# Performance work log

Hardware: AMD Instinct MI355X
Metric: run time of the kernel (lower is better)

Reference implementation:

```python
import jax, jax.numpy as jnp
import numpy as np
from jax import lax

INPUT_DIM = 1024
DICT_SIZE = 16384
K = 32
BATCH = 4096


def setup_inputs() -> dict:
    key = jax.random.key(0)
    k1, k2, k3 = jax.random.split(key, 3)
    x = jax.random.normal(k1, (BATCH, INPUT_DIM), dtype=jnp.float32)
    # kaiming-uniform-ish init for encoder
    bound_enc = float(np.sqrt(6.0 / INPUT_DIM))
    W_enc = jax.random.uniform(k2, (DICT_SIZE, INPUT_DIM), dtype=jnp.float32,
                               minval=-bound_enc, maxval=bound_enc)
    b_enc = jnp.zeros((DICT_SIZE,), dtype=jnp.float32)
    bound_dec = float(np.sqrt(6.0 / DICT_SIZE))
    W_dec = jax.random.uniform(k3, (INPUT_DIM, DICT_SIZE), dtype=jnp.float32,
                               minval=-bound_dec, maxval=bound_dec)
    # normalize decoder columns to unit norm (dim=0), as in _init_weights
    W_dec = W_dec / (jnp.linalg.norm(W_dec, axis=0, keepdims=True) + 1e-12)
    b_dec = jnp.zeros((INPUT_DIM,), dtype=jnp.float32)
    return {"x": x, "W_enc": W_enc, "b_enc": b_enc, "W_dec": W_dec, "b_dec": b_dec}


def reference(x, W_enc, b_enc, W_dec, b_dec):
    batch = x.shape[0]
    # encode: F.linear(x - b_dec, W_enc, b_enc)
    pre_acts = jnp.einsum('bi,di->bd', x - b_dec, W_enc) + b_enc  # [B, D]
    relu_acts = jnp.maximum(pre_acts, 0.0)
    # batch top-k: keep top (k * batch) activations globally
    flat = relu_acts.reshape(-1)
    total_k = min(K * batch, flat.shape[0])
    top_vals, _ = lax.top_k(flat, total_k)
    threshold = top_vals[-1]  # == kthvalue(numel - total_k + 1)
    features = relu_acts * (relu_acts >= threshold).astype(relu_acts.dtype)
    # decode: F.linear(features, W_dec, b_dec)
    reconstructed = jnp.einsum('bd,id->bi', features, W_dec) + b_dec  # [B, I]
    diff = reconstructed - x
    reconstruction_loss = jnp.mean(diff * diff)
    sparsity_loss = jnp.asarray(0.0, dtype=x.dtype)
    loss = reconstruction_loss
    l0 = jnp.mean(jnp.sum((features > 0).astype(jnp.float32), axis=-1))
    return (reconstructed, features, loss, reconstruction_loss, sparsity_loss, l0)
```

## Files before the change

### kernel.cpp

```cpp
#include <hip/hip_runtime.h>
#include <cstdint>
#include <cstddef>

#define BATCH   4096
#define INDIM   1024
#define DICT    16384
#define TOTK    (32 * 4096)
#define NFEAT   ((size_t)BATCH * DICT)
#define DELTA   3e-2f
#define BAND    0.2f
#define PS_RANK (TOTK / 32)

#define NB2       4096
#define FBINS     2048
#define HCOPIES   64
#define CAND_CAP  (1u << 19)
#define BCAP      256u
#define ZLOC_CAP  2048u
#define CLOC_CAP  3072
#define C2_CAP    65536u
#define HASH_SZ   32768u
#define ROW_CAP   512
#define ZBINS     2048

#define PSH_OFF   0ull
#define FH_OFF    16384ull
#define SCAL_OFF  32768ull
#define H1_OFF    36864ull
#define ROWC_OFF  40960ull
#define HASH_OFF  65536ull
#define FBH_OFF   524288ull
#define MEMSET0   1572864ull
#define CANDI_OFF (2ull << 20)
#define CANDB_OFF (4ull << 20)
#define C2I_OFF   (6ull << 20)
#define C2V_OFF   ((6ull << 20) + 262144)
#define ENT_OFF   (7ull << 20)
#define AHI_OFF   (24ull << 20)
#define BHI_OFF   (32ull << 20)
#define WT_OFF    (24ull << 20)
#define WS_NEED   (88ull << 20)

typedef __attribute__((ext_vector_type(8))) short short8;
typedef __attribute__((ext_vector_type(4))) float f32x4;

#define GL2LDS16(g, l) __builtin_amdgcn_global_load_lds( \
    (const __attribute__((address_space(1))) void*)(g), \
    (__attribute__((address_space(3))) void*)(l), 16, 0, 0)

__device__ inline ushort bf16_rne_u(float a) {
    unsigned u = __float_as_uint(a);
    return (ushort)((u + 0x7FFFu + ((u >> 16) & 1u)) >> 16);
}

__device__ inline float bf16_to_f(ushort u) {
    return __uint_as_float(((unsigned)u) << 16);
}

__device__ inline int fshift_calc(unsigned BL, unsigned BH) {
    const unsigned range = BH - BL;
    int s = 0;
    while ((range >> s) > (unsigned)FBINS) ++s;
    return s;
}

__global__ __launch_bounds__(256) void split_kernel(
    const float* __restrict__ x, const float* __restrict__ W,
    const float* __restrict__ b_dec,
    ushort* __restrict__ Ahi, ushort* __restrict__ Bhi)
{
    const size_t NA = (size_t)BATCH * INDIM / 4;
    const size_t NB = (size_t)DICT * INDIM / 4;
    const size_t stride = (size_t)gridDim.x * blockDim.x;
    for (size_t i = (size_t)blockIdx.x * blockDim.x + threadIdx.x; i < NA + NB; i += stride) {
        float4 v;
        ushort* hp;
        if (i < NA) {
            v = reinterpret_cast<const float4*>(x)[i];
            const float4 bd = reinterpret_cast<const float4*>(b_dec)[i & (INDIM / 4 - 1)];
            v.x -= bd.x; v.y -= bd.y; v.z -= bd.z; v.w -= bd.w;
            hp = Ahi + i * 4;
        } else {
            v = reinterpret_cast<const float4*>(W)[i - NA];
            hp = Bhi + (i - NA) * 4;
        }
        ushort4 h;
        h.x = bf16_rne_u(v.x);
        h.y = bf16_rne_u(v.y);
        h.z = bf16_rne_u(v.z);
        h.w = bf16_rne_u(v.w);
        *reinterpret_cast<ushort4*>(hp) = h;
    }
}

__global__ __launch_bounds__(256) void presample_mfma(
    const ushort* __restrict__ Ahi, const ushort* __restrict__ Bhi,
    const float* __restrict__ b_enc, unsigned* __restrict__ pshist)
{
    __shared__ __align__(16) ushort As[128 * 64];
    __shared__ __align__(16) ushort Bs[128 * 64];
    __shared__ unsigned hls[NB2];
    const int tid = threadIdx.x;
    const int lane = tid & 63, wid = tid >> 6;
    const int n0 = blockIdx.x * 128;
    const int m0 = 0;
    const int wm = wid >> 1, wn = wid & 1;

    for (int i = tid; i < NB2; i += 256) hls[i] = 0;

    f32x4 acc[4][4];
#pragma unroll
    for (int i = 0; i < 4; ++i)
#pragma unroll
        for (int j = 0; j < 4; ++j) acc[i][j] = (f32x4){0.f, 0.f, 0.f, 0.f};

    const int srow = wid * 8 + (lane >> 3);
    const int schunk = (lane & 7) ^ (lane >> 3);
    const size_t abase = (size_t)(m0 + srow) * INDIM + schunk * 8;
    const size_t bbase = (size_t)(n0 + srow) * INDIM + schunk * 8;

    for (int t = 0; t < 16; ++t) {
        const int koff = t * 64;
#pragma unroll
        for (int i = 0; i < 4; ++i) {
            GL2LDS16(Ahi + abase + koff + (size_t)i * 32 * INDIM, &As[(i * 32 + wid * 8) * 64]);
            GL2LDS16(Bhi + bbase + koff + (size_t)i * 32 * INDIM, &Bs[(i * 32 + wid * 8) * 64]);
        }
        __syncthreads();
#pragma unroll
        for (int kq2 = 0; kq2 < 2; ++kq2) {
            short8 af[4], bf[4];
#pragma unroll
            for (int f = 0; f < 4; ++f) {
                const int ra = wm * 64 + f * 16 + (lane & 15);
                const int ca = (kq2 * 4 + (lane >> 4)) ^ (ra & 7);
                af[f] = *reinterpret_cast<const short8*>(&As[ra * 64 + ca * 8]);
                const int rb = wn * 64 + f * 16 + (lane & 15);
                const int cb = (kq2 * 4 + (lane >> 4)) ^ (rb & 7);
                bf[f] = *reinterpret_cast<const short8*>(&Bs[rb * 64 + cb * 8]);
            }
#pragma unroll
            for (int fm = 0; fm < 4; ++fm)
#pragma unroll
                for (int fn = 0; fn < 4; ++fn)
                    acc[fm][fn] = __builtin_amdgcn_mfma_f32_16x16x32_bf16(
                        af[fm], bf[fn], acc[fm][fn], 0, 0, 0);
        }
        __syncthreads();
    }

    const int ccol0 = n0 + wn * 64;
#pragma unroll
    for (int fm = 0; fm < 4; ++fm) {
#pragma unroll
        for (int fn = 0; fn < 4; ++fn) {
            const int col = ccol0 + fn * 16 + (lane & 15);
            const float be = b_enc[col];
#pragma unroll
            for (int r = 0; r < 4; ++r) {
                const float val = fmaxf(acc[fm][fn][r] + be, 0.f);
                if (val > 0.f) atomicAdd(&hls[__float_as_uint(val) >> 19], 1u);
            }
        }
    }
    __syncthreads();
    for (int i = tid; i < NB2; i += 256)
        if (hls[i]) atomicAdd(&pshist[i], hls[i]);
}

__global__ __launch_bounds__(1024) void presample_find(const unsigned* __restrict__ pshist,
                                                       unsigned* __restrict__ scal)
{
    __shared__ unsigned tot[NB2];
    __shared__ unsigned tsum[1024];
    __shared__ unsigned suffix[1024];
    const int t = threadIdx.x;
    unsigned s = 0;
#pragma unroll
    for (int i = 0; i < 4; ++i) {
        const int b = t * 4 + i;
        const unsigned v = pshist[b];
        tot[b] = v;
        s += v;
    }
    tsum[t] = s;
    __syncthreads();
    if (t == 0) {
        unsigned run = 0;
        for (int i = 1023; i >= 0; --i) { suffix[i] = run; run += tsum[i]; }
    }
    __syncthreads();
    unsigned cum = suffix[t];
    for (int i = 3; i >= 0; --i) {
        const unsigned b = (unsigned)(t * 4 + i);
        const unsigned nb = cum + tot[b];
        if (cum < PS_RANK && nb >= PS_RANK) {
            const float blo = __uint_as_float(b << 19);
            const float bhi = __uint_as_float((b + 1) << 19);
            scal[20] = __float_as_uint(fmaxf(blo - BAND, 1e-30f));
            scal[21] = __float_as_uint(bhi + BAND);
        }
        cum = nb;
    }
}

__global__ __launch_bounds__(256) void encode_main(
    const ushort* __restrict__ Ahi, const ushort* __restrict__ Bhi,
    const float* __restrict__ b_enc, unsigned* __restrict__ scal,
    unsigned* __restrict__ fhist, unsigned* __restrict__ candI,
    unsigned* __restrict__ candB)
{
    __shared__ __align__(16) ushort As[128 * 64];
    __shared__ __align__(16) ushort Bs[128 * 64];
    __shared__ unsigned ci[BCAP];
    __shared__ unsigned cb[BCAP];
    __shared__ unsigned lcnt, labv, sbase;
    const int tid = threadIdx.x;
    const int lane = tid & 63, wid = tid >> 6;
    const int flat = blockIdx.y * gridDim.x + blockIdx.x;
    const int n0 = ((flat & 7) * 16 + ((flat >> 3) & 15)) * 128;
    const int m0 = (flat >> 7) * 128;
    const int wm = wid >> 1, wn = wid & 1;

    if (tid == 0) { lcnt = 0; labv = 0; }

    const unsigned BLb = scal[20], BHb = scal[21];
    const float BLf = __uint_as_float(BLb);
    const int fs = fshift_calc(BLb, BHb);

    f32x4 acc[4][4];
#pragma unroll
    for (int i = 0; i < 4; ++i)
#pragma unroll
        for (int j = 0; j < 4; ++j) acc[i][j] = (f32x4){0.f, 0.f, 0.f, 0.f};

    const int srow = wid * 8 + (lane >> 3);
    const int schunk = (lane & 7) ^ (lane >> 3);
    const size_t abase = (size_t)(m0 + srow) * INDIM + schunk * 8;
    const size_t bbase = (size_t)(n0 + srow) * INDIM + schunk * 8;

    for (int t = 0; t < 16; ++t) {
        const int koff = t * 64;
#pragma unroll
        for (int i = 0; i < 4; ++i) {
            GL2LDS16(Ahi + abase + koff + (size_t)i * 32 * INDIM, &As[(i * 32 + wid * 8) * 64]);
            GL2LDS16(Bhi + bbase + koff + (size_t)i * 32 * INDIM, &Bs[(i * 32 + wid * 8) * 64]);
        }
        __syncthreads();
#pragma unroll
        for (int kq2 = 0; kq2 < 2; ++kq2) {
            short8 af[4], bf[4];
#pragma unroll
            for (int f = 0; f < 4; ++f) {
                const int ra = wm * 64 + f * 16 + (lane & 15);
                const int ca = (kq2 * 4 + (lane >> 4)) ^ (ra & 7);
                af[f] = *reinterpret_cast<const short8*>(&As[ra * 64 + ca * 8]);
                const int rb = wn * 64 + f * 16 + (lane & 15);
                const int cbx = (kq2 * 4 + (lane >> 4)) ^ (rb & 7);
                bf[f] = *reinterpret_cast<const short8*>(&Bs[rb * 64 + cbx * 8]);
            }
#pragma unroll
            for (int fm = 0; fm < 4; ++fm)
#pragma unroll
                for (int fn = 0; fn < 4; ++fn)
                    acc[fm][fn] = __builtin_amdgcn_mfma_f32_16x16x32_bf16(
                        af[fm], bf[fn], acc[fm][fn], 0, 0, 0);
        }
        __syncthreads();
    }

    const int crow0 = m0 + wm * 64;
    const int ccol0 = n0 + wn * 64;
#pragma unroll
    for (int fm = 0; fm < 4; ++fm) {
#pragma unroll
        for (int fn = 0; fn < 4; ++fn) {
            const int col = ccol0 + fn * 16 + (lane & 15);
            const float be = b_enc[col];
#pragma unroll
            for (int r = 0; r < 4; ++r) {
                const int row = crow0 + fm * 16 + (lane >> 4) * 4 + r;
                const float val = fmaxf(acc[fm][fn][r] + be, 0.f);
                if (val >= BLf) {
                    const unsigned u = __float_as_uint(val);
                    if (u < BHb) atomicAdd(&fhist[min((u - BLb) >> fs, (unsigned)(FBINS - 1))], 1u);
                    else atomicAdd(&labv, 1u);
                    const unsigned p = atomicAdd(&lcnt, 1u);
                    if (p < BCAP) {
                        ci[p] = (unsigned)(row * DICT + col);
                        cb[p] = u;
                    }
                }
            }
        }
    }
    __syncthreads();
    if (tid == 0) {
        if (labv) atomicAdd(&scal[16], labv);
        const unsigned n = min(lcnt, BCAP);
        if (lcnt > BCAP) atomicExch(&scal[17], 1u);
        sbase = atomicAdd(&scal[2], n);
    }
    __syncthreads();
    const unsigned n = min(lcnt, BCAP);
    const unsigned gb = sbase;
    for (unsigned k = tid; k < n; k += 256) {
        const unsigned g = gb + k;
        if (g < CAND_CAP) { candI[g] = ci[k]; candB[g] = cb[k]; }
        else atomicExch(&scal[17], 1u);
    }
}

__global__ __launch_bounds__(1024) void findfine_a(const unsigned* __restrict__ fhist,
                                                   unsigned* __restrict__ scal)
{
    __shared__ unsigned fhl[FBINS];
    __shared__ unsigned tsum[1024];
    __shared__ unsigned suffix[1024];
    __shared__ unsigned sfb;
    const int t = threadIdx.x;
    fhl[t * 2] = fhist[t * 2];
    fhl[t * 2 + 1] = fhist[t * 2 + 1];
    tsum[t] = fhl[t * 2] + fhl[t * 2 + 1];
    if (t == 0) sfb = 0xFFFFFFFFu;
    __syncthreads();
    if (t == 0) {
        unsigned run = 0;
        for (int i = 1023; i >= 0; --i) { suffix[i] = run; run += tsum[i]; }
    }
    __syncthreads();
    const unsigned aboveBH = scal[16];
    unsigned cum = aboveBH + suffix[t];
    {
        const unsigned b1 = (unsigned)(t * 2 + 1);
        unsigned nb = cum + fhl[b1];
        if (cum < TOTK && nb >= TOTK) sfb = b1;
        cum = nb;
        const unsigned b0 = (unsigned)(t * 2);
        nb = cum + fhl[b0];
        if (cum < TOTK && nb >= TOTK) sfb = b0;
    }
    __syncthreads();
    if (t == 0) {
        const unsigned BLb = scal[20], BHb = scal[21];
        bool ok = (sfb != 0xFFFFFFFFu) && (scal[17] == 0u) && (scal[2] <= CAND_CAP);
        if (ok) {
            const int fs = fshift_calc(BLb, BHb);
            const unsigned flo = BLb + (sfb << fs);
            const unsigned fhi = BLb + ((sfb + 1u) << fs) - 1u;
            const float zLo = __uint_as_float(flo) - DELTA;
            const float zHi = __uint_as_float(fhi) + DELTA;
            const unsigned ZL = __float_as_uint(fmaxf(zLo, 1e-30f));
            const unsigned ZH = __float_as_uint(zHi);
            ok = ok && (ZL >= BLb);
            scal[6] = ZL;
            scal[7] = ZH;
        }
        scal[18] = ok ? 1u : 0u;
    }
}

__global__ __launch_bounds__(256) void findfine_b(const unsigned* __restrict__ candB,
                                                  const unsigned* __restrict__ candI,
                                                  unsigned* __restrict__ scal,
                                                  unsigned* __restrict__ c2idx)
{
    if (!scal[18]) return;
    __shared__ unsigned lz[ZLOC_CAP];
    __shared__ unsigned red[256];
    __shared__ unsigned lcnt, sbase;
    const int tid = threadIdx.x;
    if (tid == 0) lcnt = 0;
    __syncthreads();
    const unsigned ZL = scal[6], ZH = scal[7];
    const unsigned C = min(scal[2], CAND_CAP);
    const unsigned stride = gridDim.x * blockDim.x;
    unsigned above = 0;
    for (unsigned i = blockIdx.x * blockDim.x + tid; i < C; i += stride) {
        const unsigned u = candB[i];
        if (u > ZH) above++;
        else if (u >= ZL) {
            const unsigned p = atomicAdd(&lcnt, 1u);
            if (p < ZLOC_CAP) lz[p] = candI[i];
        }
    }
    red[tid] = above;
    __syncthreads();
    for (int s = 128; s; s >>= 1) {
        if (tid < s) red[tid] += red[tid + s];
        __syncthreads();
    }
    if (tid == 0) {
        if (red[0]) atomicAdd(&scal[8], red[0]);
        const unsigned n = min(lcnt, ZLOC_CAP);
        if (lcnt > ZLOC_CAP) { atomicExch(&scal[17], 1u); atomicExch(&scal[18], 0u); }
        sbase = atomicAdd(&scal[9], n);
    }
    __syncthreads();
    const unsigned n = min(lcnt, ZLOC_CAP);
    const unsigned gb = sbase;
    for (unsigned k = tid; k < n; k += 256) {
        const unsigned g = gb + k;
        if (g < C2_CAP) c2idx[g] = lz[k];
        else { atomicExch(&scal[17], 1u); atomicExch(&scal[18], 0u); }
    }
}

__global__ __launch_bounds__(256) void fb_encode(
    const ushort* __restrict__ Ahi, const ushort* __restrict__ Bhi,
    const float* __restrict__ b_enc, float* __restrict__ feat,
    unsigned* __restrict__ fbhist, const unsigned* __restrict__ scal)
{
    if (scal[18]) return;
    __shared__ __align__(16) ushort As[128 * 64];
    __shared__ __align__(16) ushort Bs[128 * 64];
    __shared__ unsigned hls[NB2];
    const int tid = threadIdx.x;
    const int lane = tid & 63, wid = tid >> 6;
    const int flat = blockIdx.y * gridDim.x + blockIdx.x;
    const int swz = (flat & 7) * 512 + (flat >> 3);
    const int n0 = (swz & 127) * 128;
    const int m0 = (swz >> 7) * 128;
    const int wm = wid >> 1, wn = wid & 1;

    for (int i = tid; i < NB2; i += 256) hls[i] = 0;

    f32x4 acc[4][4];
#pragma unroll
    for (int i = 0; i < 4; ++i)
#pragma unroll
        for (int j = 0; j < 4; ++j) acc[i][j] = (f32x4){0.f, 0.f, 0.f, 0.f};

    const int srow = wid * 8 + (lane >> 3);
    const int schunk = (lane & 7) ^ (lane >> 3);
    const size_t abase = (size_t)(m0 + srow) * INDIM + schunk * 8;
    const size_t bbase = (size_t)(n0 + srow) * INDIM + schunk * 8;

    for (int t = 0; t < 16; ++t) {
        const int koff = t * 64;
#pragma unroll
        for (int i = 0; i < 4; ++i) {
            GL2LDS16(Ahi + abase + koff + (size_t)i * 32 * INDIM, &As[(i * 32 + wid * 8) * 64]);
            GL2LDS16(Bhi + bbase + koff + (size_t)i * 32 * INDIM, &Bs[(i * 32 + wid * 8) * 64]);
        }
        __syncthreads();
#pragma unroll
        for (int kq2 = 0; kq2 < 2; ++kq2) {
            short8 af[4], bf[4];
#pragma unroll
            for (int f = 0; f < 4; ++f) {
                const int ra = wm * 64 + f * 16 + (lane & 15);
                const int ca = (kq2 * 4 + (lane >> 4)) ^ (ra & 7);
                af[f] = *reinterpret_cast<const short8*>(&As[ra * 64 + ca * 8]);
                const int rb = wn * 64 + f * 16 + (lane & 15);
                const int cb = (kq2 * 4 + (lane >> 4)) ^ (rb & 7);
                bf[f] = *reinterpret_cast<const short8*>(&Bs[rb * 64 + cb * 8]);
            }
#pragma unroll
            for (int fm = 0; fm < 4; ++fm)
#pragma unroll
                for (int fn = 0; fn < 4; ++fn)
                    acc[fm][fn] = __builtin_amdgcn_mfma_f32_16x16x32_bf16(
                        af[fm], bf[fn], acc[fm][fn], 0, 0, 0);
        }
        __syncthreads();
    }

    const int crow0 = m0 + wm * 64;
    const int ccol0 = n0 + wn * 64;
#pragma unroll
    for (int fm = 0; fm < 4; ++fm) {
#pragma unroll
        for (int fn = 0; fn < 4; ++fn) {
            const int col = ccol0 + fn * 16 + (lane & 15);
            const float be = b_enc[col];
#pragma unroll
            for (int r = 0; r < 4; ++r) {
                const int row = crow0 + fm * 16 + (lane >> 4) * 4 + r;
                const float val = fmaxf(acc[fm][fn][r] + be, 0.f);
                feat[(size_t)row * DICT + col] = val;
                if (val > 0.f) atomicAdd(&hls[__float_as_uint(val) >> 19], 1u);
            }
        }
    }
    __syncthreads();
    unsigned* hdst = fbhist + (size_t)(flat & (HCOPIES - 1)) * NB2;
    for (int i = tid; i < NB2; i += 256)
        if (hls[i]) atomicAdd(&hdst[i], hls[i]);
}

__global__ __launch_bounds__(1024) void fb_findbin2(const unsigned* __restrict__ fbhist,
                                                    unsigned* __restrict__ scal)
{
    if (scal[18]) return;
    __shared__ unsigned tot[NB2];
    __shared__ unsigned tsum[1024];
    __shared__ unsigned suffix[1024];
    const int t = threadIdx.x;
    if (t == 0) { scal[9] = 0; scal[8] = 0; }
    unsigned s = 0;
#pragma unroll
    for (int i = 0; i < 4; ++i) {
        const int b = t * 4 + i;
        unsigned v = 0;
        for (int c = 0; c < HCOPIES; ++c) v += fbhist[(size_t)c * NB2 + b];
        tot[b] = v;
        s += v;
    }
    tsum[t] = s;
    __syncthreads();
    if (t == 0) {
        unsigned run = 0;
        for (int i = 1023; i >= 0; --i) { suffix[i] = run; run += tsum[i]; }
    }
    __syncthreads();
    unsigned cum = suffix[t];
    for (int i = 3; i >= 0; --i) {
        const unsigned b = (unsigned)(t * 4 + i);
        const unsigned nb = cum + tot[b];
        if (cum < TOTK && nb >= TOTK) {
            scal[0] = b;
            scal[1] = cum;
            scal[10] = cum - ((b + 1 < NB2) ? tot[b + 1] : 0u);
        }
        cum = nb;
    }
}

__global__ __launch_bounds__(256) void fb_collectC(const float* __restrict__ feat,
                                                   unsigned* __restrict__ scal,
                                                   unsigned* __restrict__ candI,
                                                   unsigned* __restrict__ candB,
                                                   unsigned* __restrict__ h1)
{
    if (scal[18]) return;
    __shared__ unsigned lidx[CLOC_CAP];
    __shared__ unsigned lbits[CLOC_CAP];
    __shared__ unsigned lcnt;
    __shared__ unsigned sbase;
    const int tid = threadIdx.x;
    if (tid == 0) lcnt = 0;
    __syncthreads();
    const unsigned b = scal[0];
    const unsigned lob = (b > 0 ? b - 1 : b) << 19;
    const unsigned hib = ((b + 2 < NB2) ? (b + 2) : NB2) << 19;
    const size_t stride = (size_t)gridDim.x * blockDim.x * 4;
    size_t base = ((size_t)blockIdx.x * blockDim.x + tid) * 4;
    for (size_t i = base; i < NFEAT; i += stride) {
        const float4 v = *reinterpret_cast<const float4*>(&feat[i]);
        const unsigned u[4] = {__float_as_uint(v.x), __float_as_uint(v.y),
                               __float_as_uint(v.z), __float_as_uint(v.w)};
#pragma unroll
        for (int q = 0; q < 4; ++q) {
            if (u[q] != 0u && u[q] >= lob && u[q] < hib) {
                const unsigned p = atomicAdd(&lcnt, 1u);
                if (p < CLOC_CAP) { lidx[p] = (unsigned)(i + q); lbits[p] = u[q]; }
                if ((u[q] >> 19) == b) atomicAdd(&h1[(u[q] >> 9) & 1023u], 1u);
            }
        }
    }
    __syncthreads();
    const unsigned n = min(lcnt, (unsigned)CLOC_CAP);
    if (tid == 0) sbase = atomicAdd(&scal[24], n);
    __syncthreads();
    const unsigned gb = sbase;
    for (unsigned k = tid; k < n; k += 256) {
        const unsigned g = gb + k;
        if (g < CAND_CAP) { candI[g] = lidx[k]; candB[g] = lbits[k]; }
    }
}

__global__ __launch_bounds__(1024) void fb_selectZ(const unsigned* __restrict__ h1,
                                                   const unsigned* __restrict__ candB,
                                                   const unsigned* __restrict__ candI,
                                                   unsigned* __restrict__ scal,
                                                   unsigned* __restrict__ c2idx)
{
    if (scal[18]) return;
    __shared__ unsigned h[1024];
    __shared__ unsigned cnt[1024];
    const int t = threadIdx.x;
    h[t] = h1[t];
    __syncthreads();
    if (t == 0) {
        const unsigned b = scal[0];
        unsigned cum = scal[1];
        unsigned s = 0;
        for (int i = 1023; i >= 0; --i) {
            const unsigned nb = cum + h[i];
            if (cum < TOTK && nb >= TOTK) s = (unsigned)i;
            cum = nb;
        }
        const float slo = __uint_as_float((b << 19) | (s << 9));
        const float shi = __uint_as_float((b << 19) | (s << 9) | 0x1FFu);
        scal[6] = __float_as_uint(fmaxf(slo - DELTA, 1e-30f));
        scal[7] = __float_as_uint(shi + DELTA);
    }
    __syncthreads();
    const float ZLf = __uint_as_float(scal[6]);
    const float ZHf = __uint_as_float(scal[7]);
    const unsigned C = min(scal[24], CAND_CAP);
    unsigned above = 0;
    for (unsigned i = t; i < C; i += 1024) {
        const float v = __uint_as_float(candB[i]);
        if (v > ZHf) above++;
        else if (v >= ZLf) {
            const unsigned p = atomicAdd(&scal[9], 1u);
            if (p < C2_CAP) c2idx[p] = candI[i];
        }
    }
    cnt[t] = above;
    __syncthreads();
    for (int s2 = 512; s2; s2 >>= 1) {
        if (t < s2) cnt[t] += cnt[t + s2];
        __syncthreads();
    }
    if (t == 0) scal[8] = scal[10] + cnt[0];
}

__global__ __launch_bounds__(256) void refine2_kernel(
    const float* __restrict__ x, const float* __restrict__ W,
    const float* __restrict__ b_enc, const float* __restrict__ b_dec,
    const unsigned* __restrict__ scal, const unsigned* __restrict__ c2idx,
    float* __restrict__ c2val)
{
    const unsigned n = min(scal[9], C2_CAP);
    const size_t stride = (size_t)gridDim.x * blockDim.x;
    for (unsigned c = blockIdx.x * blockDim.x + threadIdx.x; c < n; c += stride) {
        const unsigned i = c2idx[c];
        const int m = (int)(i >> 14);
        const int d = (int)(i & (DICT - 1));
        const float* xr = x + (size_t)m * INDIM;
        const float* wr = W + (size_t)d * INDIM;
        const int kb[4] = {0, 384, 704, 1024};
        float tot = 0.f;
        for (int p = 0; p < 3; ++p) {
            float a = 0.f;
#pragma unroll 8
            for (int k = kb[p]; k < kb[p + 1]; ++k)
                a = fmaf(xr[k] - b_dec[k], wr[k], a);
            tot = (p == 0) ? a : (tot + a);
        }
        c2val[c] = tot + b_enc[d];
    }
}

__device__ inline int zone_shift(unsigned ZL, unsigned ZH) {
    const unsigned range = ZH - ZL + 1u;
    int shift = 0;
    while ((range >> shift) > (unsigned)ZBINS) ++shift;
    return shift;
}

__global__ __launch_bounds__(1024) void findv_kernel(const float* __restrict__ c2val,
                                                     unsigned* __restrict__ scal)
{
    __shared__ unsigned h[ZBINS];
    __shared__ float mem[1024];
    __shared__ unsigned mcnt;
    __shared__ unsigned sbsel, sjj;
    const int t = threadIdx.x;
    h[t] = 0;
    h[t + 1024] = 0;
    if (t == 0) mcnt = 0;
    __syncthreads();
    const unsigned n = min(scal[9], C2_CAP);
    const unsigned ZL = scal[6], ZH = scal[7];
    const int shift = zone_shift(ZL, ZH);
    for (unsigned i = t; i < n; i += 1024) {
        const unsigned bits = __float_as_uint(c2val[i]);
        const unsigned idx = (bits <= ZL) ? 0u : min((unsigned)(ZBINS - 1), (bits - ZL) >> shift);
        atomicAdd(&h[idx], 1u);
    }
    __syncthreads();
    unsigned j = TOTK - scal[8];
    if (j > n) j = n;
    if (t == 0) {
        unsigned cum = 0, bsel = 0, jj = j;
        for (int i = ZBINS - 1; i >= 0; --i) {
            const unsigned nb = cum + h[i];
            if (cum < j && nb >= j) { bsel = (unsigned)i; jj = j - cum; }
            cum = nb;
        }
        sbsel = bsel; sjj = jj;
    }
    __syncthreads();
    const unsigned bsel = sbsel, jj = sjj;
    for (unsigned i = t; i < n; i += 1024) {
        const unsigned bits = __float_as_uint(c2val[i]);
        const unsigned idx = (bits <= ZL) ? 0u : min((unsigned)(ZBINS - 1), (bits - ZL) >> shift);
        if (idx == bsel) {
            const unsigned p = atomicAdd(&mcnt, 1u);
            if (p < 1024) mem[p] = c2val[i];
        }
    }
    __syncthreads();
    const unsigned m = min(mcnt, 1024u);
    for (unsigned i = t; i < m; i += 1024) {
        const float v = mem[i];
        unsigned g = 0, eq = 0;
        for (unsigned d = 0; d < m; ++d) {
            g += (mem[d] > v) ? 1u : 0u;
            eq += (mem[d] == v) ? 1u : 0u;
        }
        if (g < jj && g + eq >= jj) scal[11] = __float_as_uint(v);
    }
}

__global__ __launch_bounds__(256) void keephash_kernel(const unsigned* __restrict__ scal,
                                                       const unsigned* __restrict__ c2idx,
                                                       const float* __restrict__ c2val,
                                                       uint2* __restrict__ hash)
{
    const unsigned n = min(scal[9], C2_CAP);
    const float vj = __uint_as_float(scal[11]);
    const unsigned stride = gridDim.x * blockDim.x;
    for (unsigned i = blockIdx.x * blockDim.x + threadIdx.x; i < n; i += stride) {
        const float v = c2val[i];
        if (v >= vj) {
            const unsigned key = c2idx[i];
            unsigned s = (key * 2654435761u) & (HASH_SZ - 1);
            while (atomicCAS(&hash[s].x, 0xFFFFFFFFu, key) != 0xFFFFFFFFu)
                s = (s + 1) & (HASH_SZ - 1);
            hash[s].y = __float_as_uint(v);
        }
    }
}

__global__ void transpose_kernel(const float* __restrict__ W, ushort* __restrict__ Wt)
{
    __shared__ float t[32][33];
    const int x0 = blockIdx.x * 32;
    const int y0 = blockIdx.y * 32;
    const int tx = threadIdx.x, ty = threadIdx.y;
    for (int r = ty; r < 32; r += 8)
        t[r][tx] = W[(size_t)(y0 + r) * DICT + x0 + tx];
    __syncthreads();
    for (int r = ty; r < 32; r += 8)
        Wt[(size_t)(x0 + r) * INDIM + y0 + tx] = bf16_rne_u(t[tx][r]);
}

__global__ __launch_bounds__(256) void scatter_kernel(
    unsigned* __restrict__ scal, const unsigned* __restrict__ candI,
    const unsigned* __restrict__ candB, const uint2* __restrict__ hash,
    float* __restrict__ feat, uint2* __restrict__ entries,
    unsigned* __restrict__ rowcnt)
{
    if (!scal[18]) return;
    __shared__ unsigned red[256];
    const unsigned C = min(scal[2], CAND_CAP);
    const unsigned ZL = scal[6], ZH = scal[7];
    const unsigned stride = gridDim.x * blockDim.x;
    unsigned kept = 0;
    for (unsigned i = blockIdx.x * blockDim.x + threadIdx.x; i < C; i += stride) {
        const unsigned u = candB[i];
        const unsigned idx = candI[i];
        float val = 0.f;
        bool keep = false;
        if (u > ZH) {
            val = __uint_as_float(u);
            keep = true;
        } else if (u >= ZL) {
            unsigned s = (idx * 2654435761u) & (HASH_SZ - 1);
            while (true) {
                const uint2 e = hash[s];
                if (e.x == idx) { val = __uint_as_float(e.y); keep = true; break; }
                if (e.x == 0xFFFFFFFFu) break;
                s = (s + 1) & (HASH_SZ - 1);
            }
        }
        if (keep) {
            feat[idx] = val;
            const unsigned row = idx >> 14;
            const unsigned p = atomicAdd(&rowcnt[row], 1u);
            if (p < ROW_CAP)
                entries[(size_t)row * ROW_CAP + p] =
                    make_uint2(idx & (DICT - 1), __float_as_uint(val));
            kept++;
        }
    }
    red[threadIdx.x] = kept;
    __syncthreads();
    for (int s = 128; s; s >>= 1) {
        if (threadIdx.x < s) red[threadIdx.x] += red[threadIdx.x + s];
        __syncthreads();
    }
    if (threadIdx.x == 0 && red[0]) atomicAdd(&scal[4], red[0]);
}

__global__ __launch_bounds__(256) void decode2_kernel(
    const unsigned* __restrict__ scal, const uint2* __restrict__ entries,
    const unsigned* __restrict__ rowcnt, const ushort* __restrict__ Wt,
    const float* __restrict__ b_dec, const float* __restrict__ x,
    float* __restrict__ recon, double* __restrict__ loss_sum)
{
    if (!scal[18]) return;
    __shared__ uint2 lst[ROW_CAP];
    __shared__ double redd[256];
    const int row = blockIdx.x;
    const int tid = threadIdx.x;
    const unsigned n = min(rowcnt[row], (unsigned)ROW_CAP);
    for (unsigned i = tid; i < n; i += 256) lst[i] = entries[(size_t)row * ROW_CAP + i];
    __syncthreads();
    float4 acc = make_float4(0.f, 0.f, 0.f, 0.f);
    for (unsigned e = 0; e < n; ++e) {
        const uint2 en = lst[e];
        const float v = __uint_as_float(en.y);
        const ushort4 w4 = *reinterpret_cast<const ushort4*>(Wt + (size_t)en.x * INDIM + tid * 4);
        acc.x = fmaf(v, bf16_to_f(w4.x), acc.x);
        acc.y = fmaf(v, bf16_to_f(w4.y), acc.y);
        acc.z = fmaf(v, bf16_to_f(w4.z), acc.z);
        acc.w = fmaf(v, bf16_to_f(w4.w), acc.w);
    }
    const float4 bd = reinterpret_cast<const float4*>(b_dec)[tid];
    acc.x += bd.x; acc.y += bd.y; acc.z += bd.z; acc.w += bd.w;
    reinterpret_cast<float4*>(recon + (size_t)row * INDIM)[tid] = acc;
    const float4 xv = reinterpret_cast<const float4*>(x + (size_t)row * INDIM)[tid];
    const double d0 = (double)acc.x - (double)xv.x;
    const double d1 = (double)acc.y - (double)xv.y;
    const double d2 = (double)acc.z - (double)xv.z;
    const double d3 = (double)acc.w - (double)xv.w;
    redd[tid] = d0 * d0 + d1 * d1 + d2 * d2 + d3 * d3;
    __syncthreads();
    for (int s = 128; s; s >>= 1) {
        if (tid < s) redd[tid] += redd[tid + s];
        __syncthreads();
    }
    if (tid == 0) atomicAdd(loss_sum, redd[0]);
}

__global__ __launch_bounds__(256) void fb_compact_decode(
    float* __restrict__ feat, unsigned* __restrict__ scal,
    const uint2* __restrict__ hash, const ushort* __restrict__ Wt,
    const float* __restrict__ b_dec, const float* __restrict__ x,
    float* __restrict__ recon, double* __restrict__ loss_sum)
{
    if (scal[18]) return;
    __shared__ uint2 lst[ROW_CAP];
    __shared__ unsigned cnt;
    __shared__ double redd[256];
    const int row = blockIdx.x;
    const int tid = threadIdx.x;
    if (tid == 0) cnt = 0;
    __syncthreads();
    const float ZLf = __uint_as_float(scal[6]);
    const float ZHf = __uint_as_float(scal[7]);
    float* frow = feat + (size_t)row * DICT;
#pragma unroll
    for (int it = 0; it < DICT / 4 / 256; ++it) {
        const int i4 = it * 256 + tid;
        float4 v = reinterpret_cast<float4*>(frow)[i4];
        float a[4] = {v.x, v.y, v.z, v.w};
        float out[4] = {0.f, 0.f, 0.f, 0.f};
#pragma unroll
        for (int q = 0; q < 4; ++q) {
            const float val = a[q];
            if (val > ZHf) {
                out[q] = val;
            } else if (val >= ZLf && val > 0.f) {
                const unsigned key = (unsigned)(row * DICT + i4 * 4 + q);
                unsigned s = (key * 2654435761u) & (HASH_SZ - 1);
                while (true) {
                    const uint2 e = hash[s];
                    if (e.x == key) { out[q] = __uint_as_float(e.y); break; }
                    if (e.x == 0xFFFFFFFFu) break;
                    s = (s + 1) & (HASH_SZ - 1);
                }
            }
            if (out[q] != 0.f) {
                const unsigned p = atomicAdd(&cnt, 1u);
                if (p < ROW_CAP)
                    lst[p] = make_uint2((unsigned)(i4 * 4 + q), __float_as_uint(out[q]));
            }
        }
        reinterpret_cast<float4*>(frow)[i4] = make_float4(out[0], out[1], out[2], out[3]);
    }
    __syncthreads();
    const unsigned n = min(cnt, (unsigned)ROW_CAP);
    float4 acc = make_float4(0.f, 0.f, 0.f, 0.f);
    for (unsigned e = 0; e < n; ++e) {
        const uint2 en = lst[e];
        const float v = __uint_as_float(en.y);
        const ushort4 w4 = *reinterpret_cast<const ushort4*>(Wt + (size_t)en.x * INDIM + tid * 4);
        acc.x = fmaf(v, bf16_to_f(w4.x), acc.x);
        acc.y = fmaf(v, bf16_to_f(w4.y), acc.y);
        acc.z = fmaf(v, bf16_to_f(w4.z), acc.z);
        acc.w = fmaf(v, bf16_to_f(w4.w), acc.w);
    }
    const float4 bd = reinterpret_cast<const float4*>(b_dec)[tid];
    acc.x += bd.x; acc.y += bd.y; acc.z += bd.z; acc.w += bd.w;
    reinterpret_cast<float4*>(recon + (size_t)row * INDIM)[tid] = acc;
    const float4 xv = reinterpret_cast<const float4*>(x + (size_t)row * INDIM)[tid];
    const double d0 = (double)acc.x - (double)xv.x;
    const double d1 = (double)acc.y - (double)xv.y;
    const double d2 = (double)acc.z - (double)xv.z;
    const double d3 = (double)acc.w - (double)xv.w;
    redd[tid] = d0 * d0 + d1 * d1 + d2 * d2 + d3 * d3;
    __syncthreads();
    for (int s = 128; s; s >>= 1) {
        if (tid < s) redd[tid] += redd[tid + s];
        __syncthreads();
    }
    if (tid == 0) {
        atomicAdd(loss_sum, redd[0]);
        if (cnt) atomicAdd(&scal[4], cnt);
    }
}

__global__ void finalize_kernel(const unsigned* __restrict__ scal, float* __restrict__ tail)
{
    const double* loss_d = reinterpret_cast<const double*>(&scal[12]);
    const float rec = (float)(loss_d[0] / (double)((size_t)BATCH * INDIM));
    tail[0] = rec;
    tail[1] = rec;
    tail[2] = 0.f;
    tail[3] = (float)scal[4] / (float)BATCH;
}

extern "C" void kernel_launch(void* const* d_in, const int* in_sizes, int n_in,
                              void* d_out, int out_size, void* d_ws, size_t ws_size,
                              hipStream_t stream)
{
    const float* x     = (const float*)d_in[0];
    const float* W_enc = (const float*)d_in[1];
    const float* b_enc = (const float*)d_in[2];
    const float* W_dec = (const float*)d_in[3];
    const float* b_dec = (const float*)d_in[4];

    float* recon = (float*)d_out;
    float* feat  = recon + (size_t)BATCH * INDIM;
    float* tail  = feat + NFEAT;

    unsigned* pshist = (unsigned*)((char*)d_ws + PSH_OFF);
    unsigned* fhist  = (unsigned*)((char*)d_ws + FH_OFF);
    unsigned* scal   = (unsigned*)((char*)d_ws + SCAL_OFF);
    unsigned* h1     = (unsigned*)((char*)d_ws + H1_OFF);
    unsigned* rowcnt = (unsigned*)((char*)d_ws + ROWC_OFF);
    uint2*    hash   = (uint2*)   ((char*)d_ws + HASH_OFF);
    unsigned* fbhist = (unsigned*)((char*)d_ws + FBH_OFF);
    unsigned* candI  = (unsigned*)((char*)d_ws + CANDI_OFF);
    unsigned* candB  = (unsigned*)((char*)d_ws + CANDB_OFF);
    unsigned* c2idx  = (unsigned*)((char*)d_ws + C2I_OFF);
    float*    c2val  = (float*)   ((char*)d_ws + C2V_OFF);
    uint2*    entries= (uint2*)   ((char*)d_ws + ENT_OFF);
    ushort*   Ahi    = (ushort*)  ((char*)d_ws + AHI_OFF);
    ushort*   Bhi    = (ushort*)  ((char*)d_ws + BHI_OFF);
    ushort*   Wt     = (ushort*)  ((char*)d_ws + WT_OFF);
    double*   loss_sum = (double*)&scal[12];

    hipMemsetAsync(d_ws, 0, MEMSET0, stream);
    hipMemsetAsync((char*)d_ws + HASH_OFF, 0xFF, HASH_SZ * sizeof(uint2), stream);
    hipMemsetAsync(feat, 0, NFEAT * sizeof(float), stream);

    split_kernel<<<2048, 256, 0, stream>>>(x, W_enc, b_dec, Ahi, Bhi);
    presample_mfma<<<128, 256, 0, stream>>>(Ahi, Bhi, b_enc, pshist);
    presample_find<<<1, 1024, 0, stream>>>(pshist, scal);
    encode_main<<<dim3(128, 32), 256, 0, stream>>>(Ahi, Bhi, b_enc, scal, fhist, candI, candB);
    findfine_a<<<1, 1024, 0, stream>>>(fhist, scal);
    findfine_b<<<256, 256, 0, stream>>>(candB, candI, scal, c2idx);

    fb_encode<<<dim3(128, 32), 256, 0, stream>>>(Ahi, Bhi, b_enc, feat, fbhist, scal);
    fb_findbin2<<<1, 1024, 0, stream>>>(fbhist, scal);
    fb_collectC<<<1024, 256, 0, stream>>>(feat, scal, candI, candB, h1);
    fb_selectZ<<<1, 1024, 0, stream>>>(h1, candB, candI, scal, c2idx);

    refine2_kernel<<<128, 256, 0, stream>>>(x, W_enc, b_enc, b_dec, scal, c2idx, c2val);
    findv_kernel<<<1, 1024, 0, stream>>>(c2val, scal);
    keephash_kernel<<<64, 256, 0, stream>>>(scal, c2idx, c2val, hash);

    transpose_kernel<<<dim3(DICT / 32, INDIM / 32), dim3(32, 8), 0, stream>>>(W_dec, Wt);

    scatter_kernel<<<256, 256, 0, stream>>>(scal, candI, candB, hash, feat, entries, rowcnt);
    decode2_kernel<<<BATCH, 256, 0, stream>>>(scal, entries, rowcnt, Wt, b_dec, x, recon, loss_sum);
    fb_compact_decode<<<BATCH, 256, 0, stream>>>(feat, scal, hash, Wt, b_dec, x, recon, loss_sum);

    finalize_kernel<<<1, 1, 0, stream>>>(scal, tail);
}
```

Before: 606.7 us.

## Fuse feature zeroing into encode epilogue and scatter zone entries directly

```diff
diff --git a/kernel.cpp b/kernel.cpp
--- a/kernel.cpp
+++ b/kernel.cpp
@@ -208,7 +208,7 @@
     const ushort* __restrict__ Ahi, const ushort* __restrict__ Bhi,
     const float* __restrict__ b_enc, unsigned* __restrict__ scal,
     unsigned* __restrict__ fhist, unsigned* __restrict__ candI,
-    unsigned* __restrict__ candB)
+    unsigned* __restrict__ candB, float* __restrict__ feat)
 {
     __shared__ __align__(16) ushort As[128 * 64];
     __shared__ __align__(16) ushort Bs[128 * 64];
@@ -281,6 +281,7 @@
             for (int r = 0; r < 4; ++r) {
                 const int row = crow0 + fm * 16 + (lane >> 4) * 4 + r;
                 const float val = fmaxf(acc[fm][fn][r] + be, 0.f);
+                feat[(size_t)row * DICT + col] = 0.f;
                 if (val >= BLf) {
                     const unsigned u = __float_as_uint(val);
                     if (u < BHb) atomicAdd(&fhist[min((u - BLb) >> fs, (unsigned)(FBINS - 1))], 1u);
@@ -712,6 +713,7 @@
                                                        const float* __restrict__ c2val,
                                                        uint2* __restrict__ hash)
 {
+    if (scal[18]) return;
     const unsigned n = min(scal[9], C2_CAP);
     const float vj = __uint_as_float(scal[11]);
     const unsigned stride = gridDim.x * blockDim.x;
@@ -742,40 +744,59 @@
 
 __global__ __launch_bounds__(256) void scatter_kernel(
     unsigned* __restrict__ scal, const unsigned* __restrict__ candI,
-    const unsigned* __restrict__ candB, const uint2* __restrict__ hash,
+    const unsigned* __restrict__ candB,
     float* __restrict__ feat, uint2* __restrict__ entries,
     unsigned* __restrict__ rowcnt)
 {
     if (!scal[18]) return;
     __shared__ unsigned red[256];
     const unsigned C = min(scal[2], CAND_CAP);
-    const unsigned ZL = scal[6], ZH = scal[7];
+    const unsigned ZH = scal[7];
     const unsigned stride = gridDim.x * blockDim.x;
     unsigned kept = 0;
     for (unsigned i = blockIdx.x * blockDim.x + threadIdx.x; i < C; i += stride) {
         const unsigned u = candB[i];
-        const unsigned idx = candI[i];
-        float val = 0.f;
-        bool keep = false;
         if (u > ZH) {
-            val = __uint_as_float(u);
-            keep = true;
-        } else if (u >= ZL) {
-            unsigned s = (idx * 2654435761u) & (HASH_SZ - 1);
-            while (true) {
-                const uint2 e = hash[s];
-                if (e.x == idx) { val = __uint_as_float(e.y); keep = true; break; }
-                if (e.x == 0xFFFFFFFFu) break;
-                s = (s + 1) & (HASH_SZ - 1);
-            }
-        }
-        if (keep) {
-            feat[idx] = val;
+            const unsigned idx = candI[i];
+            feat[idx] = __uint_as_float(u);
+            const unsigned row = idx >> 14;
+            const unsigned p = atomicAdd(&rowcnt[row], 1u);
+            if (p < ROW_CAP)
+                entries[(size_t)row * ROW_CAP + p] = make_uint2(idx & (DICT - 1), u);
+            kept++;
+        }
+    }
+    red[threadIdx.x] = kept;
+    __syncthreads();
+    for (int s = 128; s; s >>= 1) {
+        if (threadIdx.x < s) red[threadIdx.x] += red[threadIdx.x + s];
+        __syncthreads();
+    }
+    if (threadIdx.x == 0 && red[0]) atomicAdd(&scal[4], red[0]);
+}
+
+__global__ __launch_bounds__(256) void scatter_zone(
+    unsigned* __restrict__ scal, const unsigned* __restrict__ c2idx,
+    const float* __restrict__ c2val,
+    float* __restrict__ feat, uint2* __restrict__ entries,
+    unsigned* __restrict__ rowcnt)
+{
+    if (!scal[18]) return;
+    __shared__ unsigned red[256];
+    const unsigned n = min(scal[9], C2_CAP);
+    const float vj = __uint_as_float(scal[11]);
+    const unsigned stride = gridDim.x * blockDim.x;
+    unsigned kept = 0;
+    for (unsigned i = blockIdx.x * blockDim.x + threadIdx.x; i < n; i += stride) {
+        const float v = c2val[i];
+        if (v >= vj) {
+            const unsigned idx = c2idx[i];
+            feat[idx] = v;
             const unsigned row = idx >> 14;
             const unsigned p = atomicAdd(&rowcnt[row], 1u);
             if (p < ROW_CAP)
                 entries[(size_t)row * ROW_CAP + p] =
-                    make_uint2(idx & (DICT - 1), __float_as_uint(val));
+                    make_uint2(idx & (DICT - 1), __float_as_uint(v));
             kept++;
         }
     }
@@ -950,12 +971,11 @@
 
     hipMemsetAsync(d_ws, 0, MEMSET0, stream);
     hipMemsetAsync((char*)d_ws + HASH_OFF, 0xFF, HASH_SZ * sizeof(uint2), stream);
-    hipMemsetAsync(feat, 0, NFEAT * sizeof(float), stream);
 
     split_kernel<<<2048, 256, 0, stream>>>(x, W_enc, b_dec, Ahi, Bhi);
     presample_mfma<<<128, 256, 0, stream>>>(Ahi, Bhi, b_enc, pshist);
     presample_find<<<1, 1024, 0, stream>>>(pshist, scal);
-    encode_main<<<dim3(128, 32), 256, 0, stream>>>(Ahi, Bhi, b_enc, scal, fhist, candI, candB);
+    encode_main<<<dim3(128, 32), 256, 0, stream>>>(Ahi, Bhi, b_enc, scal, fhist, candI, candB, feat);
     findfine_a<<<1, 1024, 0, stream>>>(fhist, scal);
     findfine_b<<<256, 256, 0, stream>>>(candB, candI, scal, c2idx);
 
@@ -970,7 +990,8 @@
 
     transpose_kernel<<<dim3(DICT / 32, INDIM / 32), dim3(32, 8), 0, stream>>>(W_dec, Wt);
 
-    scatter_kernel<<<256, 256, 0, stream>>>(scal, candI, candB, hash, feat, entries, rowcnt);
+    scatter_kernel<<<256, 256, 0, stream>>>(scal, candI, candB, feat, entries, rowcnt);
+    scatter_zone<<<64, 256, 0, stream>>>(scal, c2idx, c2val, feat, entries, rowcnt);
     decode2_kernel<<<BATCH, 256, 0, stream>>>(scal, entries, rowcnt, Wt, b_dec, x, recon, loss_sum);
     fb_compact_decode<<<BATCH, 256, 0, stream>>>(feat, scal, hash, Wt, b_dec, x, recon, loss_sum);
 
```

Result: faster. 582.9 us (-3.9%).
